# Kernel optimization log

Measured on AMD Instinct MI355X. Metric: run time of the kernel, lower is better.

Reference implementation:

```python
import jax, jax.numpy as jnp
import numpy as np

EPS = 1e-5  # BatchNorm eps (torch default)

def conv2d(x, w, padding=0, dilation=1):
    # x: NCHW, w: OIHW
    return jax.lax.conv_general_dilated(
        x, w, window_strides=(1, 1),
        padding=[(padding, padding), (padding, padding)],
        rhs_dilation=(dilation, dilation),
        dimension_numbers=('NCHW', 'OIHW', 'NCHW'))

def bn_relu(x, scale, bias):
    # eval-mode BatchNorm with running_mean=0, running_var=1, then ReLU
    inv = scale / np.sqrt(1.0 + EPS)
    return jax.nn.relu(x * inv[None, :, None, None] + bias[None, :, None, None])

def setup_inputs() -> dict:
    key = jax.random.key(0)
    ks = jax.random.split(key, 12)
    B, C, H, W = 4, 512, 64, 64
    def nrm(k, shape, fan):
        return jax.random.normal(k, shape, jnp.float32) * np.sqrt(2.0 / fan)
    return {
        'x': jax.random.normal(ks[0], (B, C, H, W), jnp.float32),
        'w_a1': nrm(ks[1], (128, 512, 1, 1), 1 * 1 * 128),
        'w_a2': nrm(ks[2], (128, 512, 3, 3), 3 * 3 * 128),
        'w_a3': nrm(ks[3], (128, 512, 3, 3), 3 * 3 * 128),
        'w_a4': nrm(ks[4], (128, 512, 3, 3), 3 * 3 * 128),
        'w_a5': nrm(ks[5], (128, 512, 1, 1), 1 * 1 * 128),
        'bn_scale': jnp.ones((5, 128), jnp.float32),
        'bn_bias': jnp.zeros((5, 128), jnp.float32),
        'w_q': jax.random.normal(ks[6], (128, 640, 1, 1), jnp.float32) * 0.04,
        'b_q': jnp.zeros((128,), jnp.float32),
        'w_k': jax.random.normal(ks[7], (128, 640, 1, 1), jnp.float32) * 0.04,
        'b_k': jnp.zeros((128,), jnp.float32),
        'w_v': jax.random.normal(ks[8], (512, 512, 1, 1), jnp.float32) * 0.04,
        'b_v': jnp.zeros((512,), jnp.float32),
        'gamma': jax.random.uniform(ks[9], (1,), jnp.float32),
    }

def reference(x, w_a1, w_a2, w_a3, w_a4, w_a5, bn_scale, bn_bias,
              w_q, b_q, w_k, b_k, w_v, b_v, gamma):
    B, C, H, W = x.shape
    N = H * W
    # ASPP branches (query and key paths use identical weights & input,
    # so compute once and reuse — same math as the original)
    b1 = bn_relu(conv2d(x, w_a1, 0, 1), bn_scale[0], bn_bias[0])
    b2 = bn_relu(conv2d(x, w_a2, 2, 2), bn_scale[1], bn_bias[1])
    b3 = bn_relu(conv2d(x, w_a3, 3, 3), bn_scale[2], bn_bias[2])
    b4 = bn_relu(conv2d(x, w_a4, 6, 6), bn_scale[3], bn_bias[3])
    # aspp5: global avg pool -> 1x1 conv -> BN -> ReLU -> bilinear up to HxW
    # (bilinear upsample of a 1x1 map with align_corners=True is a broadcast)
    p5 = jnp.mean(x, axis=(2, 3), keepdims=True)            # [B,512,1,1]
    p5 = bn_relu(conv2d(p5, w_a5, 0, 1), bn_scale[4], bn_bias[4])
    b5 = jnp.broadcast_to(p5, (B, 128, H, W))
    feat = jnp.concatenate([b1, b2, b3, b4, b5], axis=1)    # [B,640,H,W]

    q = (conv2d(feat, w_q) + b_q[None, :, None, None]).reshape(B, 128, N)  # [B,128,N]
    k = (conv2d(feat, w_k) + b_k[None, :, None, None]).reshape(B, 128, N)  # [B,128,N]
    v = (conv2d(x, w_v) + b_v[None, :, None, None]).reshape(B, C, N)       # [B,C,N]

    energy = jnp.einsum('bcn,bcm->bnm', q, k)               # [B,N,N], unscaled
    attention = jax.nn.softmax(energy, axis=-1)
    out = jnp.einsum('bcm,bnm->bcn', v, attention).reshape(B, C, H, W)
    return gamma[0] * out + x
```

## Files before the change

kernel.cpp:

```cpp
#include <hip/hip_runtime.h>

typedef _Float16 f16x8 __attribute__((ext_vector_type(8)));
typedef _Float16 f16x4 __attribute__((ext_vector_type(4)));
typedef float f32x4 __attribute__((ext_vector_type(4)));

#define N_PIX 4096
#define C_IN  512
#define BN_INV 0.99999500003749969f
#define CCH 64

#define GLOAD_LDS16(g, l)                                        \
  __builtin_amdgcn_global_load_lds(                              \
      (const __attribute__((address_space(1))) void*)(g),        \
      (__attribute__((address_space(3))) void*)(l), 16, 0, 0)

__device__ __forceinline__ f32x4 mfma16(f16x8 a, f16x8 b, f32x4 c) {
  return __builtin_amdgcn_mfma_f32_16x16x32_f16(a, b, c, 0, 0, 0);
}
__device__ __forceinline__ f16x8 ldnt(const _Float16* base, int row, int ld, int k0, int lane) {
  return *(const f16x8*)(base + (size_t)(row + (lane & 15)) * ld + k0 + ((lane >> 4) << 3));
}

__global__ __launch_bounds__(256) void k_xT(const float* __restrict__ x, _Float16* __restrict__ xT) {
  __shared__ float t[32][33];
  int b = blockIdx.z, p0 = blockIdx.x * 32, c0 = blockIdx.y * 32;
  int tx = threadIdx.x & 31, ty = threadIdx.x >> 5;
  const float* xb = x + ((size_t)b * C_IN + c0) * N_PIX + p0;
  for (int i = 0; i < 32; i += 8) t[ty + i][tx] = xb[(size_t)(ty + i) * N_PIX + tx];
  __syncthreads();
  _Float16* o = xT + ((size_t)b * N_PIX + p0) * C_IN + c0;
  for (int i = 0; i < 32; i += 8) o[(size_t)(ty + i) * C_IN + tx] = (_Float16)t[tx][ty + i];
}

__global__ __launch_bounds__(256) void k_f2hx(const float* __restrict__ wa1, _Float16* __restrict__ w1h,
                                              const float* __restrict__ wv, _Float16* __restrict__ wvh,
                                              const float* __restrict__ wq, _Float16* __restrict__ wqh,
                                              const float* __restrict__ wk, _Float16* __restrict__ wkh) {
  int i = blockIdx.x * 256 + threadIdx.x;
  if (i < 65536) { w1h[i] = (_Float16)wa1[i]; return; }
  i -= 65536;
  if (i < 262144) { wvh[i] = (_Float16)wv[i]; return; }
  i -= 262144;
  if (i < 65536) { int oc = i >> 9, c = i & 511; wqh[i] = (_Float16)wq[oc * 640 + c]; return; }
  i -= 65536;
  if (i < 65536) { int oc = i >> 9, c = i & 511; wkh[i] = (_Float16)wk[oc * 640 + c]; }
}

__global__ __launch_bounds__(256) void k_packw(const float* __restrict__ w2, const float* __restrict__ w3,
                                               const float* __restrict__ w4, _Float16* __restrict__ wp) {
  int idx = blockIdx.x * 256 + threadIdx.x;
  int conv = idx / 589824;
  int t1 = idx % 589824;
  int tap = t1 / 65536;
  int t2 = t1 % 65536;
  int oc = t2 / 512, c = t2 % 512;
  const float* w = (conv == 0) ? w2 : (conv == 1) ? w3 : w4;
  wp[idx] = (_Float16)w[(size_t)(oc * 512 + c) * 9 + tap];
}

__global__ __launch_bounds__(256) void k_mean(const float* __restrict__ x, float* __restrict__ meanv) {
  int c = blockIdx.x, b = blockIdx.y;
  const float* p = x + ((size_t)b * C_IN + c) * N_PIX;
  float s = 0.f;
  for (int i = threadIdx.x; i < N_PIX; i += 256) s += p[i];
  for (int off = 32; off; off >>= 1) s += __shfl_down(s, off);
  __shared__ float ls[4];
  if ((threadIdx.x & 63) == 0) ls[threadIdx.x >> 6] = s;
  __syncthreads();
  if (threadIdx.x == 0) meanv[(size_t)b * C_IN + c] = (ls[0] + ls[1] + ls[2] + ls[3]) * (1.f / N_PIX);
}

__global__ void k_p5(const float* __restrict__ w5, const float* __restrict__ meanv,
                     const float* __restrict__ bnS, const float* __restrict__ bnB,
                     const float* __restrict__ wq, const float* __restrict__ bq,
                     const float* __restrict__ wk, const float* __restrict__ bk,
                     float* __restrict__ bq2, float* __restrict__ bk2) {
  __shared__ float p5s[128];
  int b = blockIdx.x, oc = threadIdx.x;
  const float* m = meanv + (size_t)b * C_IN;
  const float* w = w5 + (size_t)oc * C_IN;
  float s = 0.f;
  for (int c = 0; c < C_IN; ++c) s += w[c] * m[c];
  p5s[oc] = fmaxf(s * bnS[oc] * BN_INV + bnB[oc], 0.f);
  __syncthreads();
  float aq = bq[oc], ak = bk[oc];
  for (int c = 0; c < 128; ++c) {
    float pv = p5s[c];
    aq += wq[oc * 640 + 512 + c] * pv;
    ak += wk[oc * 640 + 512 + c] * pv;
  }
  bq2[b * 128 + oc] = aq;
  bk2[b * 128 + oc] = ak;
}

__global__ __launch_bounds__(256, 4) void k_conv(const _Float16* __restrict__ xT, const _Float16* __restrict__ w1h,
                                                 const _Float16* __restrict__ wph, const float* __restrict__ bnS,
                                                 const float* __restrict__ bnB, _Float16* __restrict__ featT) {
  __shared__ _Float16 Ap[3 * 76 * CCH];
  int y = blockIdx.x;
  int tb = blockIdx.y;
  int task = tb >> 2, b = tb & 3;
  int tid = threadIdx.x, wid = tid >> 6, lane = tid & 63;
  int dil = (task == 0) ? 0 : (task == 1) ? 2 : (task == 2) ? 3 : 6;
  int ntap = task ? 9 : 1;
  int nrow = task ? 3 : 1;
  const _Float16* wt0 = task ? wph + (size_t)(task - 1) * 9 * 128 * C_IN : w1h;
  f32x4 acc[4][2] = {};

  for (int cc = 0; cc < C_IN / CCH; ++cc) {
    int c0 = cc * CCH;
    __syncthreads();
    if (dil) {
      int nz = nrow * 2 * dil * (CCH / 8);
      for (int i = tid; i < nz; i += 256) {
        int cv = (i & (CCH / 8 - 1)) * 8;
        int t2 = i / (CCH / 8);
        int colh = t2 % (2 * dil);
        int r = t2 / (2 * dil);
        int col = (colh < dil) ? colh : 64 + colh;
        int ba = (((r * 76 + col) * CCH + cv) * 2) ^ ((col & 7) << 4);
        *(f16x8*)((char*)Ap + ba) = (f16x8){};
      }
    }
    int nf = nrow * 64 * (CCH / 8);
    for (int i = tid; i < nf; i += 256) {
      int cv = (i & (CCH / 8 - 1)) * 8;
      int t2 = i / (CCH / 8);
      int px = t2 & 63;
      int r = t2 >> 6;
      int ry = y + (r - 1) * dil;
      f16x8 v = {};
      if ((unsigned)ry < 64u)
        v = *(const f16x8*)(xT + ((size_t)b * N_PIX + ry * 64 + px) * C_IN + c0 + cv);
      int col = dil + px;
      int ba = (((r * 76 + col) * CCH + cv) * 2) ^ ((col & 7) << 4);
      *(f16x8*)((char*)Ap + ba) = v;
    }
    __syncthreads();
    for (int tap = 0; tap < ntap; ++tap) {
      int rsel = tap / 3;
      int dx = (tap % 3 - 1) * dil;
      const _Float16* wt = wt0 + (size_t)tap * 128 * C_IN;
#pragma unroll
      for (int k = 0; k < CCH / 32; ++k) {
        f16x8 wf0 = ldnt(wt, wid * 32, C_IN, c0 + k * 32, lane);
        f16x8 wf1 = ldnt(wt, wid * 32 + 16, C_IN, c0 + k * 32, lane);
        f16x8 af[4];
#pragma unroll
        for (int m = 0; m < 4; ++m) {
          int col = dil + dx + m * 16 + (lane & 15);
          int ch = k * 32 + ((lane >> 4) << 3);
          int ba = (((rsel * 76 + col) * CCH + ch) * 2) ^ ((col & 7) << 4);
          af[m] = *(const f16x8*)((char*)Ap + ba);
        }
#pragma unroll
        for (int m = 0; m < 4; ++m) {
          acc[m][0] = mfma16(af[m], wf0, acc[m][0]);
          acc[m][1] = mfma16(af[m], wf1, acc[m][1]);
        }
      }
    }
  }
  int brOff = task * 128;
  _Float16* F = featT + (size_t)b * N_PIX * 512;
#pragma unroll
  for (int n = 0; n < 2; ++n) {
    int oc = wid * 32 + n * 16 + (lane & 15);
    float inv = bnS[brOff + oc] * BN_INV, bs = bnB[brOff + oc];
#pragma unroll
    for (int m = 0; m < 4; ++m) {
#pragma unroll
      for (int r = 0; r < 4; ++r) {
        int pix = y * 64 + m * 16 + ((lane >> 4) << 2) + r;
        F[(size_t)pix * 512 + brOff + oc] = (_Float16)fmaxf(acc[m][n][r] * inv + bs, 0.f);
      }
    }
  }
}

__global__ __launch_bounds__(256) void k_qk(const _Float16* __restrict__ featT, const _Float16* __restrict__ wqh,
                                            const _Float16* __restrict__ wkh, const float* __restrict__ bq2,
                                            const float* __restrict__ bk2, _Float16* __restrict__ qT,
                                            _Float16* __restrict__ kT) {
  int b = blockIdx.z, which = blockIdx.y, p0 = blockIdx.x * 32;
  const _Float16* wh = which ? wkh : wqh;
  const float* bias = (which ? bk2 : bq2) + b * 128;
  _Float16* oT = which ? kT : qT;
  int tid = threadIdx.x, wid = tid >> 6, lane = tid & 63;
  int pw = wid & 1, ocq = wid >> 1;
  const _Float16* A = featT + (size_t)b * N_PIX * 512;
  int pr = p0 + pw * 16;
  f32x4 acc[4] = {};
  for (int kk = 0; kk < 16; ++kk) {
    f16x8 af = ldnt(A, pr, 512, kk * 32, lane);
#pragma unroll
    for (int nn = 0; nn < 4; ++nn) {
      f16x8 bf = ldnt(wh, ocq * 64 + nn * 16, 512, kk * 32, lane);
      acc[nn] = mfma16(af, bf, acc[nn]);
    }
  }
  _Float16* O = oT + (size_t)b * N_PIX * 128;
#pragma unroll
  for (int nn = 0; nn < 4; ++nn) {
    int oc = ocq * 64 + nn * 16 + (lane & 15);
    float bb = bias[oc];
#pragma unroll
    for (int r = 0; r < 4; ++r) {
      int pix = pr + ((lane >> 4) << 2) + r;
      O[(size_t)pix * 128 + oc] = (_Float16)(acc[nn][r] + bb);
    }
  }
}

__global__ __launch_bounds__(256) void k_v(const _Float16* __restrict__ xT, const _Float16* __restrict__ wvh,
                                           const float* __restrict__ bv, _Float16* __restrict__ vv) {
  int bid = blockIdx.x;
  int swz = (bid & 7) * 128 + (bid >> 3);
  int oc0 = (swz & 7) * 64;
  int p0 = ((swz >> 3) & 31) * 128;
  int b = swz >> 8;
  int tid = threadIdx.x, wid = tid >> 6, lane = tid & 63;
  const _Float16* Bm = xT + (size_t)b * N_PIX * C_IN;
  int or0 = oc0 + wid * 16;
  f32x4 acc[8] = {};
  for (int kk = 0; kk < 16; ++kk) {
    f16x8 af = ldnt(wvh, or0, C_IN, kk * 32, lane);
#pragma unroll
    for (int nn = 0; nn < 8; ++nn) {
      f16x8 bf = ldnt(Bm, p0 + nn * 16, C_IN, kk * 32, lane);
      acc[nn] = mfma16(af, bf, acc[nn]);
    }
  }
  _Float16* V = vv + (size_t)b * C_IN * N_PIX;
#pragma unroll
  for (int r = 0; r < 4; ++r) {
    int oc = or0 + ((lane >> 4) << 2) + r;
    float bb = bv[oc];
#pragma unroll
    for (int nn = 0; nn < 8; ++nn) {
      int pix = p0 + nn * 16 + (lane & 15);
      V[(size_t)oc * N_PIX + pix] = (_Float16)(acc[nn][r] + bb);
    }
  }
}

__global__ __launch_bounds__(768, 3) void k_attn(const _Float16* __restrict__ qT, const _Float16* __restrict__ kT,
                                                 const _Float16* __restrict__ vv, const float* __restrict__ x,
                                                 const float* __restrict__ gamma, float* __restrict__ out) {
  __shared__ _Float16 Kb[2][128 * 128];
  __shared__ _Float16 P[2][64 * 128];
  __shared__ float fbuf[2][64];
  __shared__ float sbuf[64];
  int bid = blockIdx.x;
  int swz = (bid & 7) * 32 + (bid >> 3);
  int n0 = (swz & 63) * 64;
  int b = swz >> 6;
  int tid = threadIdx.x, wid = tid >> 6, lane = tid & 63;
  const _Float16* Q = qT + (size_t)b * N_PIX * 128;
  const _Float16* K = kT + (size_t)b * N_PIX * 128;
  const _Float16* V = vv + (size_t)b * C_IN * N_PIX;
  float g = gamma[0];
  f16x8 qf[4];
  int n_local = (wid & 3) * 16 + (lane & 15);
  if (wid < 4) {
#pragma unroll
    for (int kk = 0; kk < 4; ++kk) qf[kk] = ldnt(Q, n0 + wid * 16, 128, kk * 32, lane);
  }
  float m_run = -3.4e38f, sm = 0.f;
  f32x4 acc[4][4];
#pragma unroll
  for (int cc = 0; cc < 4; ++cc)
#pragma unroll
    for (int nn = 0; nn < 4; ++nn) acc[cc][nn] = (f32x4){};

  auto stageK = [&](int it, int buf) {
    const _Float16* src = K + (size_t)it * 128 * 128;
    int cs = (lane & 15) << 4;
#pragma unroll
    for (int i = 0; i < 4; ++i) {
      int rr = wid * 16 + i * 4 + (lane >> 4);
      const char* gp = (const char*)(src + (size_t)rr * 128) + (cs ^ ((rr & 7) << 4));
      char* lp = (char*)&Kb[buf][0] + (size_t)(wid * 16 + i * 4) * 256;
      GLOAD_LDS16(gp, lp);
    }
  };

  auto phaseA = [&](int it) {
    int buf = it & 1;
    const char* kb = (const char*)&Kb[buf][0];
    f32x4 s8[8];
#pragma unroll
    for (int mm = 0; mm < 8; ++mm) {
      int row = mm * 16 + (lane & 15);
      int kboff = (lane >> 4) << 4;
      f32x4 s = {};
#pragma unroll
      for (int kk = 0; kk < 4; ++kk) {
        f16x8 kf = *(const f16x8*)(kb + (size_t)row * 256 + ((kk * 64 + kboff) ^ ((row & 7) << 4)));
        s = mfma16(kf, qf[kk], s);
      }
      s8[mm] = s;
    }
    float tmx = s8[0][0];
#pragma unroll
    for (int mm = 0; mm < 8; ++mm)
      tmx = fmaxf(tmx, fmaxf(fmaxf(s8[mm][0], s8[mm][1]), fmaxf(s8[mm][2], s8[mm][3])));
    tmx = fmaxf(tmx, __shfl_xor(tmx, 16));
    tmx = fmaxf(tmx, __shfl_xor(tmx, 32));
    float f = 1.f;
    if (tmx > m_run + 8.f) {
      f = __expf(m_run - tmx);
      m_run = tmx;
    }
    sm *= f;
    if (lane < 16) fbuf[buf][n_local] = f;
#pragma unroll
    for (int mm = 0; mm < 8; ++mm) {
      f16x4 pv;
#pragma unroll
      for (int r = 0; r < 4; ++r) {
        float p = __expf(s8[mm][r] - m_run);
        sm += p;
        pv[r] = (_Float16)p;
      }
      int m_local = mm * 16 + ((lane >> 4) << 2);
      *(f16x4*)((char*)&P[buf][0] + (size_t)n_local * 256 + ((m_local * 2) ^ ((n_local & 7) << 4))) = pv;
    }
  };

  auto phaseB = [&](int it) {
    int buf = it & 1;
    int c0 = (wid - 4) * 64;
    float f[4];
#pragma unroll
    for (int nn = 0; nn < 4; ++nn) f[nn] = fbuf[buf][nn * 16 + (lane & 15)];
    bool need = (f[0] != 1.f) | (f[1] != 1.f) | (f[2] != 1.f) | (f[3] != 1.f);
    if (__any(need)) {
#pragma unroll
      for (int cc = 0; cc < 4; ++cc)
#pragma unroll
        for (int nn = 0; nn < 4; ++nn) acc[cc][nn] = acc[cc][nn] * f[nn];
    }
#pragma unroll
    for (int k2 = 0; k2 < 4; ++k2) {
      f16x8 pb[4];
#pragma unroll
      for (int nn = 0; nn < 4; ++nn) {
        int n = nn * 16 + (lane & 15);
        int mbyte = k2 * 64 + ((lane >> 4) << 4);
        pb[nn] = *(const f16x8*)((char*)&P[buf][0] + (size_t)n * 256 + (mbyte ^ ((n & 7) << 4)));
      }
      __builtin_amdgcn_s_setprio(1);
#pragma unroll
      for (int cc = 0; cc < 4; ++cc) {
        f16x8 af = ldnt(V, c0 + cc * 16, N_PIX, it * 128 + k2 * 32, lane);
#pragma unroll
        for (int nn = 0; nn < 4; ++nn) acc[cc][nn] = mfma16(af, pb[nn], acc[cc][nn]);
      }
      __builtin_amdgcn_s_setprio(0);
    }
  };

  if (wid < 8) {
    stageK(0, 0);
    stageK(1, 1);
  }
  __syncthreads();
  if (wid < 4) phaseA(0);
  __syncthreads();
  for (int it = 0; it < 32; ++it) {
    if (wid < 8 && it < 30) stageK(it + 2, it & 1);
    if (wid < 4) {
      if (it < 31) phaseA(it + 1);
    } else {
      phaseB(it);
    }
    __syncthreads();
  }

  if (wid < 4) {
    float st = sm;
    st += __shfl_xor(st, 16);
    st += __shfl_xor(st, 32);
    if (lane < 16) sbuf[n_local] = st;
  }
  __syncthreads();
  if (wid >= 4) {
    int c0 = (wid - 4) * 64;
    float inv_s[4];
#pragma unroll
    for (int nn = 0; nn < 4; ++nn) inv_s[nn] = 1.f / sbuf[nn * 16 + (lane & 15)];
#pragma unroll
    for (int cc = 0; cc < 4; ++cc) {
#pragma unroll
      for (int r = 0; r < 4; ++r) {
        int oc = c0 + cc * 16 + ((lane >> 4) << 2) + r;
#pragma unroll
        for (int nn = 0; nn < 4; ++nn) {
          int pix = n0 + nn * 16 + (lane & 15);
          size_t idx = ((size_t)(b * C_IN + oc)) * N_PIX + pix;
          out[idx] = fmaf(g * inv_s[nn], acc[cc][nn][r], x[idx]);
        }
      }
    }
  }
}

extern "C" void kernel_launch(void* const* d_in, const int* in_sizes, int n_in,
                              void* d_out, int out_size, void* d_ws, size_t ws_size,
                              hipStream_t stream) {
  const float* x = (const float*)d_in[0];
  const float* wa1 = (const float*)d_in[1];
  const float* wa2 = (const float*)d_in[2];
  const float* wa3 = (const float*)d_in[3];
  const float* wa4 = (const float*)d_in[4];
  const float* wa5 = (const float*)d_in[5];
  const float* bnS = (const float*)d_in[6];
  const float* bnB = (const float*)d_in[7];
  const float* wq = (const float*)d_in[8];
  const float* bq = (const float*)d_in[9];
  const float* wk = (const float*)d_in[10];
  const float* bk = (const float*)d_in[11];
  const float* wv = (const float*)d_in[12];
  const float* bv = (const float*)d_in[13];
  const float* gamma = (const float*)d_in[14];

  char* ws = (char*)d_ws;
  size_t off = 0;
  auto alloc = [&](size_t bytes) -> char* {
    char* p = ws + off;
    off = (off + bytes + 255) & ~(size_t)255;
    return p;
  };
  _Float16* xT = (_Float16*)alloc((size_t)4 * 4096 * 512 * 2);
  _Float16* featT = (_Float16*)alloc((size_t)4 * 4096 * 512 * 2);
  _Float16* qT = (_Float16*)alloc((size_t)4 * 4096 * 128 * 2);
  _Float16* kT = (_Float16*)alloc((size_t)4 * 4096 * 128 * 2);
  _Float16* vvp = (_Float16*)alloc((size_t)4 * 512 * 4096 * 2);
  _Float16* w1h = (_Float16*)alloc((size_t)128 * 512 * 2);
  _Float16* wph = (_Float16*)alloc((size_t)3 * 9 * 128 * 512 * 2);
  _Float16* wqh = (_Float16*)alloc((size_t)128 * 512 * 2);
  _Float16* wkh = (_Float16*)alloc((size_t)128 * 512 * 2);
  _Float16* wvh = (_Float16*)alloc((size_t)512 * 512 * 2);
  float* meanv = (float*)alloc((size_t)4 * 512 * 4);
  float* bq2 = (float*)alloc((size_t)4 * 128 * 4);
  float* bk2 = (float*)alloc((size_t)4 * 128 * 4);
  if (off > ws_size) return;

  float* out = (float*)d_out;

  hipLaunchKernelGGL(k_xT, dim3(128, 16, 4), dim3(256), 0, stream, x, xT);
  hipLaunchKernelGGL(k_f2hx, dim3(1792), dim3(256), 0, stream, wa1, w1h, wv, wvh, wq, wqh, wk, wkh);
  hipLaunchKernelGGL(k_packw, dim3(6912), dim3(256), 0, stream, wa2, wa3, wa4, wph);
  hipLaunchKernelGGL(k_mean, dim3(512, 4), dim3(256), 0, stream, x, meanv);
  hipLaunchKernelGGL(k_p5, dim3(4), dim3(128), 0, stream, wa5, meanv, bnS + 4 * 128, bnB + 4 * 128,
                     wq, bq, wk, bk, bq2, bk2);
  hipLaunchKernelGGL(k_conv, dim3(64, 16), dim3(256), 0, stream, xT, w1h, wph, bnS, bnB, featT);
  hipLaunchKernelGGL(k_qk, dim3(128, 2, 4), dim3(256), 0, stream, featT, wqh, wkh, bq2, bk2, qT, kT);
  hipLaunchKernelGGL(k_v, dim3(1024), dim3(256), 0, stream, xT, wvh, bv, vvp);
  hipLaunchKernelGGL(k_attn, dim3(256), dim3(768), 0, stream, qT, kT, vvp, x, gamma, out);
}
```

Measured before the change: 415.2 us.

## Compute two output rows per conv block and move K staging to PV waves

The ASPP conv kernel now computes two image rows per block, halving the channel chunk to 32 so the doubled row-band LDS tile stays about the same size. Each weight fragment loaded from global memory is reused across twice as many MFMAs, which cuts weight traffic, at the cost of more accumulator registers and half as many blocks in the grid. In the attention kernel, K-tile staging moves from waves 0-7 to waves 4-11, the PV waves, so the QK-energy waves no longer issue loads. This is meant to shorten the energy phase's critical path.

```diff
diff --git a/kernel.cpp b/kernel.cpp
--- a/kernel.cpp
+++ b/kernel.cpp
@@ -7,7 +7,7 @@
 #define N_PIX 4096
 #define C_IN  512
 #define BN_INV 0.99999500003749969f
-#define CCH 64
+#define CCH 32
 
 #define GLOAD_LDS16(g, l)                                        \
   __builtin_amdgcn_global_load_lds(                              \
@@ -96,29 +96,29 @@
 __global__ __launch_bounds__(256, 4) void k_conv(const _Float16* __restrict__ xT, const _Float16* __restrict__ w1h,
                                                  const _Float16* __restrict__ wph, const float* __restrict__ bnS,
                                                  const float* __restrict__ bnB, _Float16* __restrict__ featT) {
-  __shared__ _Float16 Ap[3 * 76 * CCH];
-  int y = blockIdx.x;
+  __shared__ _Float16 Ap[6 * 76 * CCH];
+  int y0 = blockIdx.x * 2;
   int tb = blockIdx.y;
   int task = tb >> 2, b = tb & 3;
   int tid = threadIdx.x, wid = tid >> 6, lane = tid & 63;
   int dil = (task == 0) ? 0 : (task == 1) ? 2 : (task == 2) ? 3 : 6;
   int ntap = task ? 9 : 1;
-  int nrow = task ? 3 : 1;
+  int nrow = task ? 6 : 2;
   const _Float16* wt0 = task ? wph + (size_t)(task - 1) * 9 * 128 * C_IN : w1h;
-  f32x4 acc[4][2] = {};
+  f32x4 acc[8][2] = {};
 
   for (int cc = 0; cc < C_IN / CCH; ++cc) {
     int c0 = cc * CCH;
     __syncthreads();
     if (dil) {
-      int nz = nrow * 2 * dil * (CCH / 8);
+      int nz = 6 * 2 * dil * (CCH / 8);
       for (int i = tid; i < nz; i += 256) {
         int cv = (i & (CCH / 8 - 1)) * 8;
         int t2 = i / (CCH / 8);
         int colh = t2 % (2 * dil);
-        int r = t2 / (2 * dil);
+        int rband = t2 / (2 * dil);
         int col = (colh < dil) ? colh : 64 + colh;
-        int ba = (((r * 76 + col) * CCH + cv) * 2) ^ ((col & 7) << 4);
+        int ba = (((rband * 76 + col) * CCH + cv) * 2) ^ ((col & 7) << 4);
         *(f16x8*)((char*)Ap + ba) = (f16x8){};
       }
     }
@@ -127,37 +127,31 @@
       int cv = (i & (CCH / 8 - 1)) * 8;
       int t2 = i / (CCH / 8);
       int px = t2 & 63;
-      int r = t2 >> 6;
-      int ry = y + (r - 1) * dil;
+      int rband = t2 >> 6;
+      int ry = y0 + (rband & 1) + ((rband >> 1) - 1) * dil;
       f16x8 v = {};
       if ((unsigned)ry < 64u)
         v = *(const f16x8*)(xT + ((size_t)b * N_PIX + ry * 64 + px) * C_IN + c0 + cv);
       int col = dil + px;
-      int ba = (((r * 76 + col) * CCH + cv) * 2) ^ ((col & 7) << 4);
+      int ba = (((rband * 76 + col) * CCH + cv) * 2) ^ ((col & 7) << 4);
       *(f16x8*)((char*)Ap + ba) = v;
     }
     __syncthreads();
     for (int tap = 0; tap < ntap; ++tap) {
-      int rsel = tap / 3;
+      int band = tap / 3;
       int dx = (tap % 3 - 1) * dil;
       const _Float16* wt = wt0 + (size_t)tap * 128 * C_IN;
-#pragma unroll
-      for (int k = 0; k < CCH / 32; ++k) {
-        f16x8 wf0 = ldnt(wt, wid * 32, C_IN, c0 + k * 32, lane);
-        f16x8 wf1 = ldnt(wt, wid * 32 + 16, C_IN, c0 + k * 32, lane);
-        f16x8 af[4];
-#pragma unroll
-        for (int m = 0; m < 4; ++m) {
-          int col = dil + dx + m * 16 + (lane & 15);
-          int ch = k * 32 + ((lane >> 4) << 3);
-          int ba = (((rsel * 76 + col) * CCH + ch) * 2) ^ ((col & 7) << 4);
-          af[m] = *(const f16x8*)((char*)Ap + ba);
-        }
-#pragma unroll
-        for (int m = 0; m < 4; ++m) {
-          acc[m][0] = mfma16(af[m], wf0, acc[m][0]);
-          acc[m][1] = mfma16(af[m], wf1, acc[m][1]);
-        }
+      f16x8 wf0 = ldnt(wt, wid * 32, C_IN, c0, lane);
+      f16x8 wf1 = ldnt(wt, wid * 32 + 16, C_IN, c0, lane);
+#pragma unroll
+      for (int m = 0; m < 8; ++m) {
+        int rband = band * 2 + (m >> 2);
+        int col = dil + dx + (m & 3) * 16 + (lane & 15);
+        int ch = (lane >> 4) << 3;
+        int ba = (((rband * 76 + col) * CCH + ch) * 2) ^ ((col & 7) << 4);
+        f16x8 af = *(const f16x8*)((char*)Ap + ba);
+        acc[m][0] = mfma16(af, wf0, acc[m][0]);
+        acc[m][1] = mfma16(af, wf1, acc[m][1]);
       }
     }
   }
@@ -168,10 +162,10 @@
     int oc = wid * 32 + n * 16 + (lane & 15);
     float inv = bnS[brOff + oc] * BN_INV, bs = bnB[brOff + oc];
 #pragma unroll
-    for (int m = 0; m < 4; ++m) {
+    for (int m = 0; m < 8; ++m) {
 #pragma unroll
       for (int r = 0; r < 4; ++r) {
-        int pix = y * 64 + m * 16 + ((lane >> 4) << 2) + r;
+        int pix = (y0 + (m >> 2)) * 64 + (m & 3) * 16 + ((lane >> 4) << 2) + r;
         F[(size_t)pix * 512 + brOff + oc] = (_Float16)fmaxf(acc[m][n][r] * inv + bs, 0.f);
       }
     }
@@ -275,12 +269,13 @@
 
   auto stageK = [&](int it, int buf) {
     const _Float16* src = K + (size_t)it * 128 * 128;
+    int w8 = wid - 4;
     int cs = (lane & 15) << 4;
 #pragma unroll
     for (int i = 0; i < 4; ++i) {
-      int rr = wid * 16 + i * 4 + (lane >> 4);
+      int rr = w8 * 16 + i * 4 + (lane >> 4);
       const char* gp = (const char*)(src + (size_t)rr * 128) + (cs ^ ((rr & 7) << 4));
-      char* lp = (char*)&Kb[buf][0] + (size_t)(wid * 16 + i * 4) * 256;
+      char* lp = (char*)&Kb[buf][0] + (size_t)(w8 * 16 + i * 4) * 256;
       GLOAD_LDS16(gp, lp);
     }
   };
@@ -361,7 +356,7 @@
     }
   };
 
-  if (wid < 8) {
+  if (wid >= 4) {
     stageK(0, 0);
     stageK(1, 1);
   }
@@ -369,10 +364,10 @@
   if (wid < 4) phaseA(0);
   __syncthreads();
   for (int it = 0; it < 32; ++it) {
-    if (wid < 8 && it < 30) stageK(it + 2, it & 1);
     if (wid < 4) {
       if (it < 31) phaseA(it + 1);
     } else {
+      if (it < 30) stageK(it + 2, it & 1);
       phaseB(it);
     }
     __syncthreads();
@@ -455,7 +450,7 @@
   hipLaunchKernelGGL(k_mean, dim3(512, 4), dim3(256), 0, stream, x, meanv);
   hipLaunchKernelGGL(k_p5, dim3(4), dim3(128), 0, stream, wa5, meanv, bnS + 4 * 128, bnB + 4 * 128,
                      wq, bq, wk, bk, bq2, bk2);
-  hipLaunchKernelGGL(k_conv, dim3(64, 16), dim3(256), 0, stream, xT, w1h, wph, bnS, bnB, featT);
+  hipLaunchKernelGGL(k_conv, dim3(32, 16), dim3(256), 0, stream, xT, w1h, wph, bnS, bnB, featT);
   hipLaunchKernelGGL(k_qk, dim3(128, 2, 4), dim3(256), 0, stream, featT, wqh, wkh, bq2, bk2, qT, kT);
   hipLaunchKernelGGL(k_v, dim3(1024), dim3(256), 0, stream, xT, wvh, bv, vvp);
   hipLaunchKernelGGL(k_attn, dim3(256), dim3(768), 0, stream, qT, kT, vvp, x, gamma, out);
```

New measurement: 415.8 us. Within noise of the previous version (+0.1%).
